# Kernel tuning notes

Measured on AMD Instinct MI355X. Metric: run time of the kernel, lower is better.

Reference implementation:

```python
import jax, jax.numpy as jnp
import numpy as np

B, E, D, M = 128, 8, 512, 4
H = M * D


def setup_inputs() -> dict:
    key = jax.random.key(0)
    k = jax.random.split(key, 6)
    scale1 = 1.0 / np.sqrt(D)
    scale2 = 1.0 / np.sqrt(H)
    return {
        "features": jax.random.normal(k[0], (B, E, D), jnp.float32),
        "target_features": jax.random.normal(k[1], (B, E, D), jnp.float32),
        # batched params for the E x E grid of 2-layer MLPs
        "W1": jax.random.uniform(k[2], (E, E, D, H), jnp.float32, -scale1, scale1),
        "b1": jax.random.uniform(k[3], (E, E, H), jnp.float32, -scale1, scale1),
        "W2": jax.random.uniform(k[4], (E, E, H, D), jnp.float32, -scale2, scale2),
        "b2": jax.random.uniform(k[5], (E, E, D), jnp.float32, -scale2, scale2),
    }


def reference(features, target_features, W1, b1, W2, b2):
    # adapter (a, e) is applied to features[:, a]; all E^2 MLPs batched as grouped GEMMs
    # h: [B, A=E(adapted), E(inner), H]
    h = jax.nn.gelu(jnp.einsum('bad,aedh->baeh', features, W1) + b1, approximate=False)
    out = jnp.einsum('baeh,aehd->baed', h, W2) + b2  # [B, A, E, D]
    # per-(a,e) MSE against target_features[:, a], summed over grid, / num_experts
    err = out - target_features[:, :, None, :]
    per_pair_mse = jnp.mean(err * err, axis=(0, 3))  # [A, E]
    return jnp.sum(per_pair_mse) / E
```

## Files before the change

### kernel.cpp

```cpp
#include <hip/hip_runtime.h>
#include <math.h>


typedef float floatx4 __attribute__((ext_vector_type(4)));
typedef __bf16 bf16x8 __attribute__((ext_vector_type(8)));
typedef unsigned short ushortx8 __attribute__((ext_vector_type(8)));
typedef unsigned short ushortx4 __attribute__((ext_vector_type(4)));

__device__ __forceinline__ unsigned short f2bf(float f) {
    unsigned u = __builtin_bit_cast(unsigned, f);
    u += 0x7fffu + ((u >> 16) & 1u);
    return (unsigned short)(u >> 16);
}

#define LDSTR 40

__global__ __launch_bounds__(256, 3) void k_gemm1(
    const float* __restrict__ feat, const float* __restrict__ W1,
    const float* __restrict__ b1, unsigned short* __restrict__ hbuf)
{
    __shared__ __align__(16) unsigned short lA[128 * LDSTR];
    __shared__ __align__(16) unsigned short lB[128 * LDSTR];

    const int bi = blockIdx.x;
    const int xcd = bi & 7, slot = bi >> 3;
    const int pair = xcd * 8 + (slot >> 4);
    const int nt   = slot & 15;
    const int a    = pair >> 3;
    const int t = threadIdx.x;
    const int w = t >> 6, l = t & 63;
    const int lr = l & 15, lq = l >> 4;
    const int n_base = nt * 128;

    const float* Bp = W1 + (size_t)pair * 512 * 2048 + n_base;
    const int ar = t >> 3;
    const int ac = (t & 7) * 4;
    const int bk0 = w * 8;

    floatx4 apf[4];
    float bpf[16];

    auto loadA = [&](int kb) {
        #pragma unroll
        for (int s = 0; s < 4; ++s) {
            const float* p = feat + ((size_t)((ar + 32 * s) * 8 + a)) * 512 + kb + ac;
            apf[s] = *(const floatx4*)p;
        }
    };
    auto loadB = [&](int kb) {
        #pragma unroll
        for (int rep = 0; rep < 2; ++rep)
            #pragma unroll
            for (int jj = 0; jj < 8; ++jj)
                bpf[rep * 8 + jj] = Bp[(size_t)(kb + bk0 + jj) * 2048 + rep * 64 + l];
    };
    auto stage = [&]() {
        #pragma unroll
        for (int s = 0; s < 4; ++s) {
            ushortx4 v = { f2bf(apf[s][0]), f2bf(apf[s][1]),
                           f2bf(apf[s][2]), f2bf(apf[s][3]) };
            *(ushortx4*)&lA[(ar + 32 * s) * LDSTR + ac] = v;
        }
        #pragma unroll
        for (int rep = 0; rep < 2; ++rep) {
            ushortx8 v;
            #pragma unroll
            for (int jj = 0; jj < 8; ++jj) v[jj] = f2bf(bpf[rep * 8 + jj]);
            *(ushortx8*)&lB[(rep * 64 + l) * LDSTR + bk0] = v;
        }
    };

    const int m0 = (w & 1) * 64;
    const int n0 = (w >> 1) * 64;
    floatx4 acc[4][4];
    const floatx4 zero = {0.f, 0.f, 0.f, 0.f};
    #pragma unroll
    for (int i = 0; i < 4; ++i)
        #pragma unroll
        for (int j = 0; j < 4; ++j) acc[i][j] = zero;

    loadA(0); loadB(0);
    for (int kt = 0; kt < 16; ++kt) {
        __syncthreads();
        stage();
        __syncthreads();
        if (kt + 1 < 16) { loadA((kt + 1) * 32); loadB((kt + 1) * 32); }
        bf16x8 af[4], bv[4];
        #pragma unroll
        for (int i = 0; i < 4; ++i)
            af[i] = __builtin_bit_cast(bf16x8,
                *(const ushortx8*)&lA[(m0 + 16 * i + lr) * LDSTR + lq * 8]);
        #pragma unroll
        for (int j = 0; j < 4; ++j)
            bv[j] = __builtin_bit_cast(bf16x8,
                *(const ushortx8*)&lB[(n0 + 16 * j + lr) * LDSTR + lq * 8]);
        #pragma unroll
        for (int i = 0; i < 4; ++i)
            #pragma unroll
            for (int j = 0; j < 4; ++j)
                acc[i][j] = __builtin_amdgcn_mfma_f32_16x16x32_bf16(
                    af[i], bv[j], acc[i][j], 0, 0, 0);
    }

    #pragma unroll
    for (int j = 0; j < 4; ++j) {
        const int col = n_base + n0 + 16 * j + lr;
        const float bias = b1[pair * 2048 + col];
        const size_t cbase = ((size_t)pair * 64 + (col >> 5)) * 128;
        const int cw = col & 31;
        #pragma unroll
        for (int i = 0; i < 4; ++i)
            #pragma unroll
            for (int r = 0; r < 4; ++r) {
                const int row = m0 + 16 * i + lq * 4 + r;
                float x = acc[i][j][r] + bias;
                float g = 0.5f * x * (1.0f + erff(x * 0.70710678118654752f));
                hbuf[(cbase + row) * 32 + cw] = f2bf(g);
            }
    }
}

__global__ __launch_bounds__(256, 2) void k_gemm2(
    const unsigned short* __restrict__ hbuf, const float* __restrict__ W2,
    const float* __restrict__ b2, const float* __restrict__ tgt,
    float* __restrict__ partials)
{
    __shared__ __align__(16) unsigned short lA[128 * LDSTR];
    __shared__ __align__(16) unsigned short lB[64 * LDSTR];
    __shared__ float red[4];

    const int bi = blockIdx.x;
    const int xcd = bi & 7, slot = bi >> 3;
    const int pair = xcd * 8 + (slot >> 3);
    const int nt   = slot & 7;
    const int a    = pair >> 3;
    const int t = threadIdx.x;
    const int w = t >> 6, l = t & 63;
    const int lr = l & 15, lq = l >> 4;
    const int n_base = nt * 64;

    const float* Bp = W2 + (size_t)pair * 2048 * 512 + n_base;
    const unsigned short* Ap = hbuf + (size_t)pair * 64 * 4096 + t * 16;
    const int bk0 = w * 8;

    ushortx8 apf[2];
    float bpf[8];

    auto loadA = [&](int kt) {
        const unsigned short* p = Ap + (size_t)kt * 4096;
        apf[0] = *(const ushortx8*)p;
        apf[1] = *(const ushortx8*)(p + 8);
    };
    auto loadB = [&](int kb) {
        #pragma unroll
        for (int jj = 0; jj < 8; ++jj)
            bpf[jj] = Bp[(size_t)(kb + bk0 + jj) * 512 + l];
    };
    auto stage = [&]() {
        *(ushortx8*)&lA[(t >> 1) * LDSTR + (t & 1) * 16] = apf[0];
        *(ushortx8*)&lA[(t >> 1) * LDSTR + (t & 1) * 16 + 8] = apf[1];
        ushortx8 v;
        #pragma unroll
        for (int jj = 0; jj < 8; ++jj) v[jj] = f2bf(bpf[jj]);
        *(ushortx8*)&lB[l * LDSTR + bk0] = v;
    };

    const int m0 = (w & 1) * 64;
    const int n0 = (w >> 1) * 32;
    floatx4 acc[4][2];
    const floatx4 zero = {0.f, 0.f, 0.f, 0.f};
    #pragma unroll
    for (int i = 0; i < 4; ++i)
        #pragma unroll
        for (int j = 0; j < 2; ++j) acc[i][j] = zero;

    loadA(0); loadB(0);
    for (int kt = 0; kt < 64; ++kt) {
        __syncthreads();
        stage();
        __syncthreads();
        if (kt + 1 < 64) { loadA(kt + 1); loadB((kt + 1) * 32); }
        bf16x8 af[4], bv[2];
        #pragma unroll
        for (int i = 0; i < 4; ++i)
            af[i] = __builtin_bit_cast(bf16x8,
                *(const ushortx8*)&lA[(m0 + 16 * i + lr) * LDSTR + lq * 8]);
        #pragma unroll
        for (int j = 0; j < 2; ++j)
            bv[j] = __builtin_bit_cast(bf16x8,
                *(const ushortx8*)&lB[(n0 + 16 * j + lr) * LDSTR + lq * 8]);
        #pragma unroll
        for (int i = 0; i < 4; ++i)
            #pragma unroll
            for (int j = 0; j < 2; ++j)
                acc[i][j] = __builtin_amdgcn_mfma_f32_16x16x32_bf16(
                    af[i], bv[j], acc[i][j], 0, 0, 0);
    }

    float lsum = 0.f;
    #pragma unroll
    for (int j = 0; j < 2; ++j) {
        const int col = n_base + n0 + 16 * j + lr;
        const float bias = b2[pair * 512 + col];
        #pragma unroll
        for (int i = 0; i < 4; ++i)
            #pragma unroll
            for (int r = 0; r < 4; ++r) {
                const int row = m0 + 16 * i + lq * 4 + r;
                float e = acc[i][j][r] + bias - tgt[((size_t)row * 8 + a) * 512 + col];
                lsum += e * e;
            }
    }
    #pragma unroll
    for (int off = 32; off > 0; off >>= 1) lsum += __shfl_down(lsum, off, 64);
    if (l == 0) red[w] = lsum;
    __syncthreads();
    if (t == 0) partials[bi] = red[0] + red[1] + red[2] + red[3];
}

__global__ void k_reduce(const float* __restrict__ partials, float* __restrict__ out)
{
    const int t = threadIdx.x;
    float v = partials[t];
    #pragma unroll
    for (int off = 32; off > 0; off >>= 1) v += __shfl_down(v, off, 64);
    __shared__ float red[8];
    if ((t & 63) == 0) red[t >> 6] = v;
    __syncthreads();
    if (t == 0) {
        float s = 0.f;
        #pragma unroll
        for (int i = 0; i < 8; ++i) s += red[i];
        out[0] = s * (1.0f / 524288.0f);
    }
}

extern "C" void kernel_launch(void* const* d_in, const int* in_sizes, int n_in,
                              void* d_out, int out_size, void* d_ws, size_t ws_size,
                              hipStream_t stream) {
    const float* feat = (const float*)d_in[0];
    const float* tgt  = (const float*)d_in[1];
    const float* W1   = (const float*)d_in[2];
    const float* b1   = (const float*)d_in[3];
    const float* W2   = (const float*)d_in[4];
    const float* b2   = (const float*)d_in[5];

    unsigned short* hbuf = (unsigned short*)d_ws;
    float* partials = (float*)((char*)d_ws + (size_t)33554432);
    float* out = (float*)d_out;

    k_gemm1<<<dim3(1024), dim3(256), 0, stream>>>(feat, W1, b1, hbuf);
    k_gemm2<<<dim3(512),  dim3(256), 0, stream>>>(hbuf, W2, b2, tgt, partials);
    k_reduce<<<dim3(1),   dim3(512), 0, stream>>>(partials, out);
}
```

Baseline: 548.9 us.

## Double-buffer B tiles, load A fragments directly from global, single barrier per step

Both GEMM kernels now double-buffer the B tile in LDS with a two-stage register prefetch, so each k-step needs one barrier instead of two. The A operand is no longer staged through LDS: gemm1 reads features straight from global and converts them to bf16 in registers, and gemm2 reads the bf16 hidden tile directly into MFMA fragments. Weight loads become nontemporal (using float2 in gemm1), and MFMA blocks are wrapped in s_setprio. The aim is to cut LDS traffic and barrier stalls and to hide global latency. The cost is higher register pressure and redundant global reads of A across waves.

```diff
diff --git a/kernel.cpp b/kernel.cpp
--- a/kernel.cpp
+++ b/kernel.cpp
@@ -3,9 +3,9 @@
 
 
 typedef float floatx4 __attribute__((ext_vector_type(4)));
+typedef float floatx2 __attribute__((ext_vector_type(2)));
 typedef __bf16 bf16x8 __attribute__((ext_vector_type(8)));
 typedef unsigned short ushortx8 __attribute__((ext_vector_type(8)));
-typedef unsigned short ushortx4 __attribute__((ext_vector_type(4)));
 
 __device__ __forceinline__ unsigned short f2bf(float f) {
     unsigned u = __builtin_bit_cast(unsigned, f);
@@ -13,14 +13,18 @@
     return (unsigned short)(u >> 16);
 }
 
+__device__ __forceinline__ void barrier_nd() {
+    asm volatile("s_waitcnt lgkmcnt(0)" ::: "memory");
+    __builtin_amdgcn_s_barrier();
+}
+
 #define LDSTR 40
 
 __global__ __launch_bounds__(256, 3) void k_gemm1(
     const float* __restrict__ feat, const float* __restrict__ W1,
     const float* __restrict__ b1, unsigned short* __restrict__ hbuf)
 {
-    __shared__ __align__(16) unsigned short lA[128 * LDSTR];
-    __shared__ __align__(16) unsigned short lB[128 * LDSTR];
+    __shared__ __align__(16) unsigned short lB[2][128 * LDSTR];
 
     const int bi = blockIdx.x;
     const int xcd = bi & 7, slot = bi >> 3;
@@ -31,47 +35,35 @@
     const int w = t >> 6, l = t & 63;
     const int lr = l & 15, lq = l >> 4;
     const int n_base = nt * 128;
-
-    const float* Bp = W1 + (size_t)pair * 512 * 2048 + n_base;
-    const int ar = t >> 3;
-    const int ac = (t & 7) * 4;
-    const int bk0 = w * 8;
-
-    floatx4 apf[4];
-    float bpf[16];
-
-    auto loadA = [&](int kb) {
-        #pragma unroll
-        for (int s = 0; s < 4; ++s) {
-            const float* p = feat + ((size_t)((ar + 32 * s) * 8 + a)) * 512 + kb + ac;
-            apf[s] = *(const floatx4*)p;
-        }
-    };
-    auto loadB = [&](int kb) {
-        #pragma unroll
-        for (int rep = 0; rep < 2; ++rep)
-            #pragma unroll
-            for (int jj = 0; jj < 8; ++jj)
-                bpf[rep * 8 + jj] = Bp[(size_t)(kb + bk0 + jj) * 2048 + rep * 64 + l];
-    };
-    auto stage = [&]() {
-        #pragma unroll
-        for (int s = 0; s < 4; ++s) {
-            ushortx4 v = { f2bf(apf[s][0]), f2bf(apf[s][1]),
-                           f2bf(apf[s][2]), f2bf(apf[s][3]) };
-            *(ushortx4*)&lA[(ar + 32 * s) * LDSTR + ac] = v;
-        }
-        #pragma unroll
-        for (int rep = 0; rep < 2; ++rep) {
-            ushortx8 v;
-            #pragma unroll
-            for (int jj = 0; jj < 8; ++jj) v[jj] = f2bf(bpf[rep * 8 + jj]);
-            *(ushortx8*)&lB[(rep * 64 + l) * LDSTR + bk0] = v;
-        }
-    };
-
     const int m0 = (w & 1) * 64;
     const int n0 = (w >> 1) * 64;
+
+    const float* Bp = W1 + (size_t)pair * 512 * 2048 + n_base + 2 * l;
+    const int bk0 = w * 8;
+    const float* Af = feat + ((size_t)(m0 + lr) * 8 + a) * 512 + lq * 8;
+
+    floatx2 bpf0[8], bpf1[8];
+
+#define G1_LOADB(KT, S)                                                        \
+    {                                                                          \
+        _Pragma("unroll")                                                      \
+        for (int jj = 0; jj < 8; ++jj)                                         \
+            S[jj] = __builtin_nontemporal_load(                                \
+                (const floatx2*)(Bp + (size_t)((KT) * 32 + bk0 + jj) * 2048)); \
+    }
+
+#define G1_STAGEB(S, BUF)                                                      \
+    {                                                                          \
+        ushortx8 v0, v1;                                                       \
+        _Pragma("unroll")                                                      \
+        for (int jj = 0; jj < 8; ++jj) {                                       \
+            v0[jj] = f2bf(S[jj][0]);                                           \
+            v1[jj] = f2bf(S[jj][1]);                                           \
+        }                                                                      \
+        *(ushortx8*)&lB[BUF][(2 * l) * LDSTR + bk0] = v0;                      \
+        *(ushortx8*)&lB[BUF][(2 * l + 1) * LDSTR + bk0] = v1;                  \
+    }
+
     floatx4 acc[4][4];
     const floatx4 zero = {0.f, 0.f, 0.f, 0.f};
     #pragma unroll
@@ -79,27 +71,53 @@
         #pragma unroll
         for (int j = 0; j < 4; ++j) acc[i][j] = zero;
 
-    loadA(0); loadB(0);
-    for (int kt = 0; kt < 16; ++kt) {
-        __syncthreads();
-        stage();
-        __syncthreads();
-        if (kt + 1 < 16) { loadA((kt + 1) * 32); loadB((kt + 1) * 32); }
-        bf16x8 af[4], bv[4];
-        #pragma unroll
-        for (int i = 0; i < 4; ++i)
-            af[i] = __builtin_bit_cast(bf16x8,
-                *(const ushortx8*)&lA[(m0 + 16 * i + lr) * LDSTR + lq * 8]);
-        #pragma unroll
-        for (int j = 0; j < 4; ++j)
-            bv[j] = __builtin_bit_cast(bf16x8,
-                *(const ushortx8*)&lB[(n0 + 16 * j + lr) * LDSTR + lq * 8]);
-        #pragma unroll
-        for (int i = 0; i < 4; ++i)
-            #pragma unroll
-            for (int j = 0; j < 4; ++j)
-                acc[i][j] = __builtin_amdgcn_mfma_f32_16x16x32_bf16(
-                    af[i], bv[j], acc[i][j], 0, 0, 0);
+    G1_LOADB(0, bpf0)
+    G1_LOADB(1, bpf1)
+    G1_STAGEB(bpf0, 0)
+    barrier_nd();
+
+#define G1_BODY(KT, BUF, SLD, SST, GLD, GST)                                   \
+    {                                                                          \
+        bf16x8 bv[4];                                                          \
+        _Pragma("unroll")                                                      \
+        for (int j = 0; j < 4; ++j)                                            \
+            bv[j] = __builtin_bit_cast(bf16x8,                                 \
+                *(const ushortx8*)&lB[BUF][(n0 + 16 * j + lr) * LDSTR + lq * 8]); \
+        floatx4 a0[4], a1[4];                                                  \
+        _Pragma("unroll")                                                      \
+        for (int i = 0; i < 4; ++i) {                                          \
+            const float* p = Af + (size_t)(65536 * i) + (KT) * 32;             \
+            a0[i] = *(const floatx4*)p;                                        \
+            a1[i] = *(const floatx4*)(p + 4);                                  \
+        }                                                                      \
+        if (GLD) G1_LOADB((KT) + 2, SLD)                                       \
+        bf16x8 af[4];                                                          \
+        _Pragma("unroll")                                                      \
+        for (int i = 0; i < 4; ++i) {                                          \
+            ushortx8 v;                                                        \
+            _Pragma("unroll")                                                  \
+            for (int r = 0; r < 4; ++r) {                                      \
+                v[r] = f2bf(a0[i][r]);                                         \
+                v[4 + r] = f2bf(a1[i][r]);                                     \
+            }                                                                  \
+            af[i] = __builtin_bit_cast(bf16x8, v);                             \
+        }                                                                      \
+        __builtin_amdgcn_s_setprio(1);                                         \
+        _Pragma("unroll")                                                      \
+        for (int i = 0; i < 4; ++i)                                            \
+            _Pragma("unroll")                                                  \
+            for (int j = 0; j < 4; ++j)                                        \
+                acc[i][j] = __builtin_amdgcn_mfma_f32_16x16x32_bf16(           \
+                    af[i], bv[j], acc[i][j], 0, 0, 0);                         \
+        __builtin_amdgcn_s_setprio(0);                                         \
+        if (GST) G1_STAGEB(SST, (BUF) ^ 1)                                     \
+        barrier_nd();                                                          \
+    }
+
+    #pragma unroll 1
+    for (int kt = 0; kt < 16; kt += 2) {
+        G1_BODY(kt,     0, bpf0, bpf1, (kt + 2 < 16), 1)
+        G1_BODY(kt + 1, 1, bpf1, bpf0, (kt + 3 < 16), (kt + 2 < 16))
     }
 
     #pragma unroll
@@ -118,6 +136,9 @@
                 hbuf[(cbase + row) * 32 + cw] = f2bf(g);
             }
     }
+#undef G1_LOADB
+#undef G1_STAGEB
+#undef G1_BODY
 }
 
 __global__ __launch_bounds__(256, 2) void k_gemm2(
@@ -125,8 +146,7 @@
     const float* __restrict__ b2, const float* __restrict__ tgt,
     float* __restrict__ partials)
 {
-    __shared__ __align__(16) unsigned short lA[128 * LDSTR];
-    __shared__ __align__(16) unsigned short lB[64 * LDSTR];
+    __shared__ __align__(16) unsigned short lB[2][64 * LDSTR];
     __shared__ float red[4];
 
     const int bi = blockIdx.x;
@@ -138,35 +158,40 @@
     const int w = t >> 6, l = t & 63;
     const int lr = l & 15, lq = l >> 4;
     const int n_base = nt * 64;
-
-    const float* Bp = W2 + (size_t)pair * 2048 * 512 + n_base;
-    const unsigned short* Ap = hbuf + (size_t)pair * 64 * 4096 + t * 16;
-    const int bk0 = w * 8;
-
-    ushortx8 apf[2];
-    float bpf[8];
-
-    auto loadA = [&](int kt) {
-        const unsigned short* p = Ap + (size_t)kt * 4096;
-        apf[0] = *(const ushortx8*)p;
-        apf[1] = *(const ushortx8*)(p + 8);
-    };
-    auto loadB = [&](int kb) {
-        #pragma unroll
-        for (int jj = 0; jj < 8; ++jj)
-            bpf[jj] = Bp[(size_t)(kb + bk0 + jj) * 512 + l];
-    };
-    auto stage = [&]() {
-        *(ushortx8*)&lA[(t >> 1) * LDSTR + (t & 1) * 16] = apf[0];
-        *(ushortx8*)&lA[(t >> 1) * LDSTR + (t & 1) * 16 + 8] = apf[1];
-        ushortx8 v;
-        #pragma unroll
-        for (int jj = 0; jj < 8; ++jj) v[jj] = f2bf(bpf[jj]);
-        *(ushortx8*)&lB[l * LDSTR + bk0] = v;
-    };
-
     const int m0 = (w & 1) * 64;
     const int n0 = (w >> 1) * 32;
+
+    const float* Bp = W2 + (size_t)pair * 2048 * 512 + n_base + l;
+    const int bk0 = w * 8;
+    const unsigned short* Ahp = hbuf + (size_t)pair * 262144
+                              + (size_t)(m0 + lr) * 32 + lq * 8;
+
+    float bpf0[8], bpf1[8];
+    ushortx8 apf0[4], apf1[4];
+
+#define G2_LOADB(KT, S)                                                        \
+    {                                                                          \
+        _Pragma("unroll")                                                      \
+        for (int jj = 0; jj < 8; ++jj)                                         \
+            S[jj] = __builtin_nontemporal_load(                               \
+                Bp + (size_t)((KT) * 32 + bk0 + jj) * 512);                    \
+    }
+
+#define G2_LOADA(KT, S)                                                        \
+    {                                                                          \
+        _Pragma("unroll")                                                      \
+        for (int i = 0; i < 4; ++i)                                            \
+            S[i] = *(const ushortx8*)(Ahp + (size_t)(KT) * 4096 + i * 512);    \
+    }
+
+#define G2_STAGEB(S, BUF)                                                      \
+    {                                                                          \
+        ushortx8 v;                                                            \
+        _Pragma("unroll")                                                      \
+        for (int jj = 0; jj < 8; ++jj) v[jj] = f2bf(S[jj]);                    \
+        *(ushortx8*)&lB[BUF][l * LDSTR + bk0] = v;                             \
+    }
+
     floatx4 acc[4][2];
     const floatx4 zero = {0.f, 0.f, 0.f, 0.f};
     #pragma unroll
@@ -174,27 +199,39 @@
         #pragma unroll
         for (int j = 0; j < 2; ++j) acc[i][j] = zero;
 
-    loadA(0); loadB(0);
-    for (int kt = 0; kt < 64; ++kt) {
-        __syncthreads();
-        stage();
-        __syncthreads();
-        if (kt + 1 < 64) { loadA(kt + 1); loadB((kt + 1) * 32); }
-        bf16x8 af[4], bv[2];
-        #pragma unroll
-        for (int i = 0; i < 4; ++i)
-            af[i] = __builtin_bit_cast(bf16x8,
-                *(const ushortx8*)&lA[(m0 + 16 * i + lr) * LDSTR + lq * 8]);
-        #pragma unroll
-        for (int j = 0; j < 2; ++j)
-            bv[j] = __builtin_bit_cast(bf16x8,
-                *(const ushortx8*)&lB[(n0 + 16 * j + lr) * LDSTR + lq * 8]);
-        #pragma unroll
-        for (int i = 0; i < 4; ++i)
-            #pragma unroll
-            for (int j = 0; j < 2; ++j)
-                acc[i][j] = __builtin_amdgcn_mfma_f32_16x16x32_bf16(
-                    af[i], bv[j], acc[i][j], 0, 0, 0);
+    G2_LOADB(0, bpf0)
+    G2_LOADB(1, bpf1)
+    G2_LOADA(0, apf0)
+    G2_LOADA(1, apf1)
+    G2_STAGEB(bpf0, 0)
+    barrier_nd();
+
+#define G2_BODY(KT, BUF, SLD, SST, APF, GLD, GST)                              \
+    {                                                                          \
+        bf16x8 bv[2];                                                          \
+        _Pragma("unroll")                                                      \
+        for (int j = 0; j < 2; ++j)                                            \
+            bv[j] = __builtin_bit_cast(bf16x8,                                 \
+                *(const ushortx8*)&lB[BUF][(n0 + 16 * j + lr) * LDSTR + lq * 8]); \
+        if (GLD) G2_LOADB((KT) + 2, SLD)                                       \
+        __builtin_amdgcn_s_setprio(1);                                         \
+        _Pragma("unroll")                                                      \
+        for (int i = 0; i < 4; ++i)                                            \
+            _Pragma("unroll")                                                  \
+            for (int j = 0; j < 2; ++j)                                        \
+                acc[i][j] = __builtin_amdgcn_mfma_f32_16x16x32_bf16(           \
+                    __builtin_bit_cast(bf16x8, APF[i]), bv[j],                 \
+                    acc[i][j], 0, 0, 0);                                       \
+        __builtin_amdgcn_s_setprio(0);                                         \
+        if (GLD) G2_LOADA((KT) + 2, APF)                                       \
+        if (GST) G2_STAGEB(SST, (BUF) ^ 1)                                     \
+        barrier_nd();                                                          \
+    }
+
+    #pragma unroll 1
+    for (int kt = 0; kt < 64; kt += 2) {
+        G2_BODY(kt,     0, bpf0, bpf1, apf0, (kt + 2 < 64), 1)
+        G2_BODY(kt + 1, 1, bpf1, bpf0, apf1, (kt + 3 < 64), (kt + 2 < 64))
     }
 
     float lsum = 0.f;
@@ -216,6 +253,10 @@
     if (l == 0) red[w] = lsum;
     __syncthreads();
     if (t == 0) partials[bi] = red[0] + red[1] + red[2] + red[3];
+#undef G2_LOADB
+#undef G2_LOADA
+#undef G2_STAGEB
+#undef G2_BODY
 }
 
 __global__ void k_reduce(const float* __restrict__ partials, float* __restrict__ out)
```

Result: slower. 562.8 us (+2.5%).
